# Performance work log

Hardware: AMD Instinct MI355X
Metric: run time of the kernel (lower is better)

The kernel has to match this reference:

```python
import jax, jax.numpy as jnp
import numpy as np

N, H, G, D, FF, R = 16384, 32, 8, 128, 2, 4
GROUPS = H // G            # n_head = heads per kv group
NBAND = D // (2 * FF)      # 32


def _fold_k(t):
    # t: [N, G, D] -> (real, imag) each [N, NBAND, G*FF]; mirrors torch transpose/reshape order
    Df = D // 2
    t = jnp.swapaxes(t, -1, -2)  # [N, D, G]
    def fold(x):  # x: [N, Df, G]
        x = x.reshape(-1, NBAND, FF, G)
        x = jnp.swapaxes(x, 1, 2)          # [N, FF, NBAND, G]
        return x.reshape(-1, NBAND, G * FF)
    return fold(t[:, :Df, :]), fold(t[:, Df:, :])


def _fold_q(t):
    # t: [N, H, D] -> (real, imag) each [N, GROUPS, NBAND, G*FF]
    Df = D // 2
    t = t.reshape(-1, G, GROUPS, D).transpose(0, 2, 1, 3)  # [N, GROUPS, G, D]
    t = jnp.swapaxes(t, -1, -2)                            # [N, GROUPS, D, G]
    def fold(x):  # x: [N, GROUPS, Df, G]
        x = x.reshape(-1, GROUPS, NBAND, FF, G)
        x = jnp.swapaxes(x, 2, 3)                          # [N, GROUPS, FF, NBAND, G]
        return x.reshape(-1, GROUPS, NBAND, G * FF)
    return fold(t[:, :, :Df, :]), fold(t[:, :, Df:, :])


def setup_inputs() -> dict:
    key = jax.random.key(0)
    ks = jax.random.split(key, 5)
    return {
        "q": jax.random.normal(ks[0], (N, H, D), jnp.float32),
        "k": jax.random.normal(ks[1], (N, G, D), jnp.float32),
        "v": jax.random.normal(ks[2], (N, G, D), jnp.float32),
        "qk_index_proj": 0.02 * jax.random.normal(ks[3], (NBAND, G * FF, FF), jnp.float32),
        "v_transform": 0.02 * jax.random.normal(ks[4], (H, D, R), jnp.float32),
    }


def reference(q, k, v, qk_index_proj, v_transform):
    # index_k: fold K, project per-band, concat real/imag -> [N, D]
    kr_re, kr_im = _fold_k(k)
    kr_re_p = jnp.einsum('bnf,nfr->bnr', kr_re, qk_index_proj)
    kr_im_p = jnp.einsum('bnf,nfr->bnr', kr_im, qk_index_proj)
    index_k = jnp.concatenate(
        [kr_re_p.reshape(-1, NBAND * FF), kr_im_p.reshape(-1, NBAND * FF)], axis=-1)

    # index_q: fold Q, project per-band, concat real/imag -> [N, GROUPS, D]
    qr_re, qr_im = _fold_q(q)
    qr_re_p = jnp.einsum('tgnf,nfr->tgnr', qr_re, qk_index_proj)
    qr_im_p = jnp.einsum('tgnf,nfr->tgnr', qr_im, qk_index_proj)
    index_q = jnp.concatenate(
        [qr_re_p.reshape(-1, GROUPS, NBAND * FF), qr_im_p.reshape(-1, GROUPS, NBAND * FF)], axis=-1)

    # weights: low-rank V transform + L2 norm -> [N, GROUPS]
    v_h = jnp.repeat(v, GROUPS, axis=1)                     # [N, H, D]
    w = jnp.einsum('nhd,hdr->nhr', v_h, v_transform)        # [N, H, R]
    w = w.reshape(-1, G, GROUPS, R).transpose(0, 2, 1, 3).reshape(-1, GROUPS, G * R)
    weights = jnp.linalg.norm(w.astype(jnp.float32), axis=-1)
    return index_q, index_k, weights
```

## Files before the change

### kernel.cpp

```cpp
#include <hip/hip_runtime.h>

#define NN 16384
#define HH 32
#define GG 8
#define DD 128
#define RR 4
#define NGROUPS 4
#define NBAND 32


__global__ __launch_bounds__(256) void idxer_kernel(
    const float* __restrict__ q, const float* __restrict__ k,
    const float* __restrict__ v, const float* __restrict__ proj,
    const float* __restrict__ vt, float* __restrict__ out)
{
    const int b = blockIdx.x;
    const int tid = threadIdx.x;

    __shared__ float sq[HH * DD];
    __shared__ float sk[GG * DD];
    __shared__ float sv[GG * DD];
    __shared__ float sproj[NBAND * 33];
    __shared__ float sw[HH];

    {
        const float4* q4 = (const float4*)(q + (size_t)b * (HH * DD));
        float4* s4 = (float4*)sq;
        #pragma unroll
        for (int i = 0; i < 4; ++i) s4[tid + 256 * i] = q4[tid + 256 * i];
        const float4* k4 = (const float4*)(k + (size_t)b * (GG * DD));
        ((float4*)sk)[tid] = k4[tid];
        const float4* v4 = (const float4*)(v + (size_t)b * (GG * DD));
        ((float4*)sv)[tid] = v4[tid];
        #pragma unroll
        for (int i = 0; i < 4; ++i) {
            int p = tid + 256 * i;
            sproj[(p >> 5) * 33 + (p & 31)] = proj[p];
        }
    }
    __syncthreads();

    {
        const int group = tid >> 6;
        const int im = (tid >> 5) & 1;
        const int n = tid & 31;
        const int dbase = (n & 15) * 4 + (n >> 4) + im * 64;
        float acc0 = 0.f, acc1 = 0.f;
        #pragma unroll
        for (int j = 0; j < 16; ++j) {
            const int d = dbase + (j >> 3) * 2;
            const int head = (j & 7) * 4 + group;
            const float qv = sq[head * DD + d];
            acc0 += qv * sproj[n * 33 + j * 2];
            acc1 += qv * sproj[n * 33 + j * 2 + 1];
        }
        float2* o2 = (float2*)out;
        o2[(size_t)b * 256 + group * 64 + im * 32 + n] = make_float2(acc0, acc1);
    }

    if (tid < 64) {
        const int im = tid >> 5;
        const int n = tid & 31;
        const int dbase = (n & 15) * 4 + (n >> 4) + im * 64;
        float acc0 = 0.f, acc1 = 0.f;
        #pragma unroll
        for (int j = 0; j < 16; ++j) {
            const int d = dbase + (j >> 3) * 2;
            const int g = j & 7;
            const float kv = sk[g * DD + d];
            acc0 += kv * sproj[n * 33 + j * 2];
            acc1 += kv * sproj[n * 33 + j * 2 + 1];
        }
        float2* o2 = (float2*)(out + (size_t)NN * 512);
        o2[(size_t)b * 64 + im * 32 + n] = make_float2(acc0, acc1);
    }

    {
        const int h = tid >> 3;
        const int s = tid & 7;
        const int g = h >> 2;
        const float4* vt4 = (const float4*)vt;
        float a0 = 0.f, a1 = 0.f, a2 = 0.f, a3 = 0.f;
        #pragma unroll
        for (int i = 0; i < 16; ++i) {
            const int d = i * 8 + s;
            const float4 w4 = vt4[h * DD + d];
            const float vv = sv[g * DD + d];
            a0 += vv * w4.x; a1 += vv * w4.y; a2 += vv * w4.z; a3 += vv * w4.w;
        }
        #pragma unroll
        for (int off = 4; off >= 1; off >>= 1) {
            a0 += __shfl_down(a0, off, 8);
            a1 += __shfl_down(a1, off, 8);
            a2 += __shfl_down(a2, off, 8);
            a3 += __shfl_down(a3, off, 8);
        }
        if (s == 0) sw[h] = a0 * a0 + a1 * a1 + a2 * a2 + a3 * a3;
    }
    __syncthreads();

    if (tid < NGROUPS) {
        float acc = 0.f;
        #pragma unroll
        for (int g = 0; g < 8; ++g) acc += sw[g * 4 + tid];
        out[(size_t)NN * 512 + (size_t)NN * 128 + (size_t)b * 4 + tid] = sqrtf(acc);
    }
}

extern "C" void kernel_launch(void* const* d_in, const int* in_sizes, int n_in,
                              void* d_out, int out_size, void* d_ws, size_t ws_size,
                              hipStream_t stream) {
    const float* q    = (const float*)d_in[0];
    const float* k    = (const float*)d_in[1];
    const float* v    = (const float*)d_in[2];
    const float* proj = (const float*)d_in[3];
    const float* vt   = (const float*)d_in[4];
    float* out = (float*)d_out;
    idxer_kernel<<<NN, 256, 0, stream>>>(q, k, v, proj, vt, out);
}
```

Measured before the change: 448.3 us.

## Process four tokens per block with register-resident projection and direct global loads

Each block now handles four tokens instead of one. The projection weights are held in registers, loaded once per thread and reused across tokens. Q and K are read straight from global memory instead of being staged through shared memory, and the V-transform weights are loaded once and applied to all four tokens. The aim is less shared-memory staging, fewer barriers and less redundant weight traffic per token, at the cost of more registers per thread and strided, uncoalesced global reads of q.

Measured after the change: 560.9 us. 25.1% more time.

```diff
diff --git a/kernel.cpp b/kernel.cpp
--- a/kernel.cpp
+++ b/kernel.cpp
@@ -7,103 +7,131 @@
 #define RR 4
 #define NGROUPS 4
 #define NBAND 32
+#define TPB 4
 
 
-__global__ __launch_bounds__(256) void idxer_kernel(
+__global__ __launch_bounds__(256, 4) void idxer_kernel(
     const float* __restrict__ q, const float* __restrict__ k,
     const float* __restrict__ v, const float* __restrict__ proj,
     const float* __restrict__ vt, float* __restrict__ out)
 {
-    const int b = blockIdx.x;
+    const int b0  = blockIdx.x * TPB;
     const int tid = threadIdx.x;
+    const int im  = (tid >> 5) & 1;
+    const int n   = tid & 31;
+    const int wav = tid >> 6;
 
-    __shared__ float sq[HH * DD];
-    __shared__ float sk[GG * DD];
-    __shared__ float sv[GG * DD];
-    __shared__ float sproj[NBAND * 33];
-    __shared__ float sw[HH];
+    __shared__ float sv[TPB * GG * DD];
+    __shared__ float sw[TPB * HH];
+
+    float pr[32];
+    {
+        const float4* proj4 = (const float4*)proj;
+        #pragma unroll
+        for (int jj = 0; jj < 8; ++jj) {
+            const float4 t = proj4[n * 8 + jj];
+            pr[jj * 4 + 0] = t.x; pr[jj * 4 + 1] = t.y;
+            pr[jj * 4 + 2] = t.z; pr[jj * 4 + 3] = t.w;
+        }
+    }
+
+    float4 vreg[4];
+    {
+        const float4* v4 = (const float4*)(v + (size_t)b0 * (GG * DD));
+        #pragma unroll
+        for (int i = 0; i < 4; ++i) vreg[i] = v4[tid + 256 * i];
+    }
+
+    const int dbase = (n & 15) * 4 + (n >> 4) + im * 64;
 
     {
-        const float4* q4 = (const float4*)(q + (size_t)b * (HH * DD));
-        float4* s4 = (float4*)sq;
+        float2* oq2 = (float2*)out;
         #pragma unroll
-        for (int i = 0; i < 4; ++i) s4[tid + 256 * i] = q4[tid + 256 * i];
-        const float4* k4 = (const float4*)(k + (size_t)b * (GG * DD));
-        ((float4*)sk)[tid] = k4[tid];
-        const float4* v4 = (const float4*)(v + (size_t)b * (GG * DD));
-        ((float4*)sv)[tid] = v4[tid];
-        #pragma unroll
-        for (int i = 0; i < 4; ++i) {
-            int p = tid + 256 * i;
-            sproj[(p >> 5) * 33 + (p & 31)] = proj[p];
+        for (int t = 0; t < TPB; ++t) {
+            const float* qb = q + (size_t)(b0 + t) * (HH * DD);
+            float a0 = 0.f, a1 = 0.f;
+            #pragma unroll
+            for (int jj = 0; jj < 8; ++jj) {
+                const int head = jj * 4 + wav;
+                const float q0 = qb[head * DD + dbase];
+                const float q1 = qb[head * DD + dbase + 2];
+                a0 += q0 * pr[2 * jj];
+                a1 += q0 * pr[2 * jj + 1];
+                a0 += q1 * pr[2 * (jj + 8)];
+                a1 += q1 * pr[2 * (jj + 8) + 1];
+            }
+            oq2[(size_t)(b0 + t) * 256 + wav * 64 + im * 32 + n] =
+                make_float2(a0, a1);
         }
     }
-    __syncthreads();
 
     {
-        const int group = tid >> 6;
-        const int im = (tid >> 5) & 1;
-        const int n = tid & 31;
-        const int dbase = (n & 15) * 4 + (n >> 4) + im * 64;
-        float acc0 = 0.f, acc1 = 0.f;
+        const float* kb = k + (size_t)(b0 + wav) * (GG * DD);
+        float a0 = 0.f, a1 = 0.f;
         #pragma unroll
-        for (int j = 0; j < 16; ++j) {
-            const int d = dbase + (j >> 3) * 2;
-            const int head = (j & 7) * 4 + group;
-            const float qv = sq[head * DD + d];
-            acc0 += qv * sproj[n * 33 + j * 2];
-            acc1 += qv * sproj[n * 33 + j * 2 + 1];
+        for (int jj = 0; jj < 8; ++jj) {
+            const float k0 = kb[jj * DD + dbase];
+            const float k1 = kb[jj * DD + dbase + 2];
+            a0 += k0 * pr[2 * jj];
+            a1 += k0 * pr[2 * jj + 1];
+            a0 += k1 * pr[2 * (jj + 8)];
+            a1 += k1 * pr[2 * (jj + 8) + 1];
         }
-        float2* o2 = (float2*)out;
-        o2[(size_t)b * 256 + group * 64 + im * 32 + n] = make_float2(acc0, acc1);
+        float2* ok2 = (float2*)(out + (size_t)NN * 512);
+        ok2[(size_t)(b0 + wav) * 64 + im * 32 + n] = make_float2(a0, a1);
     }
 
-    if (tid < 64) {
-        const int im = tid >> 5;
-        const int n = tid & 31;
-        const int dbase = (n & 15) * 4 + (n >> 4) + im * 64;
-        float acc0 = 0.f, acc1 = 0.f;
+    {
+        float4* s4 = (float4*)sv;
         #pragma unroll
-        for (int j = 0; j < 16; ++j) {
-            const int d = dbase + (j >> 3) * 2;
-            const int g = j & 7;
-            const float kv = sk[g * DD + d];
-            acc0 += kv * sproj[n * 33 + j * 2];
-            acc1 += kv * sproj[n * 33 + j * 2 + 1];
-        }
-        float2* o2 = (float2*)(out + (size_t)NN * 512);
-        o2[(size_t)b * 64 + im * 32 + n] = make_float2(acc0, acc1);
+        for (int i = 0; i < 4; ++i) s4[tid + 256 * i] = vreg[i];
     }
+    __syncthreads();
 
     {
         const int h = tid >> 3;
         const int s = tid & 7;
         const int g = h >> 2;
         const float4* vt4 = (const float4*)vt;
-        float a0 = 0.f, a1 = 0.f, a2 = 0.f, a3 = 0.f;
+        float acc[TPB][4];
+        #pragma unroll
+        for (int t = 0; t < TPB; ++t)
+            acc[t][0] = acc[t][1] = acc[t][2] = acc[t][3] = 0.f;
         #pragma unroll
         for (int i = 0; i < 16; ++i) {
             const int d = i * 8 + s;
             const float4 w4 = vt4[h * DD + d];
-            const float vv = sv[g * DD + d];
-            a0 += vv * w4.x; a1 += vv * w4.y; a2 += vv * w4.z; a3 += vv * w4.w;
+            #pragma unroll
+            for (int t = 0; t < TPB; ++t) {
+                const float vv = sv[t * (GG * DD) + g * DD + d];
+                acc[t][0] += vv * w4.x; acc[t][1] += vv * w4.y;
+                acc[t][2] += vv * w4.z; acc[t][3] += vv * w4.w;
+            }
         }
         #pragma unroll
-        for (int off = 4; off >= 1; off >>= 1) {
-            a0 += __shfl_down(a0, off, 8);
-            a1 += __shfl_down(a1, off, 8);
-            a2 += __shfl_down(a2, off, 8);
-            a3 += __shfl_down(a3, off, 8);
+        for (int t = 0; t < TPB; ++t) {
+            #pragma unroll
+            for (int off = 4; off >= 1; off >>= 1) {
+                acc[t][0] += __shfl_down(acc[t][0], off, 8);
+                acc[t][1] += __shfl_down(acc[t][1], off, 8);
+                acc[t][2] += __shfl_down(acc[t][2], off, 8);
+                acc[t][3] += __shfl_down(acc[t][3], off, 8);
+            }
+            if (s == 0)
+                sw[t * HH + h] = acc[t][0] * acc[t][0] + acc[t][1] * acc[t][1]
+                               + acc[t][2] * acc[t][2] + acc[t][3] * acc[t][3];
         }
-        if (s == 0) sw[h] = a0 * a0 + a1 * a1 + a2 * a2 + a3 * a3;
     }
     __syncthreads();
 
-    if (tid < NGROUPS) {
+    if (tid < TPB * NGROUPS) {
+        const int t = tid >> 2;
+        const int grp = tid & 3;
         float acc = 0.f;
         #pragma unroll
-        for (int g = 0; g < 8; ++g) acc += sw[g * 4 + tid];
-        out[(size_t)NN * 512 + (size_t)NN * 128 + (size_t)b * 4 + tid] = sqrtf(acc);
+        for (int g8 = 0; g8 < 8; ++g8) acc += sw[t * HH + g8 * 4 + grp];
+        out[(size_t)NN * 512 + (size_t)NN * 128 + (size_t)(b0 + t) * 4 + grp] =
+            sqrtf(acc);
     }
 }
 
@@ -116,5 +144,5 @@
     const float* proj = (const float*)d_in[3];
     const float* vt   = (const float*)d_in[4];
     float* out = (float*)d_out;
-    idxer_kernel<<<NN, 256, 0, stream>>>(q, k, v, proj, vt, out);
+    idxer_kernel<<<NN / TPB, 256, 0, stream>>>(q, k, v, proj, vt, out);
 }
```
